# Optimization experiments

Hardware: AMD Instinct MI355X
Metric: run time of the kernel (lower is better)

The kernel has to match this reference:

```python
import jax, jax.numpy as jnp
import numpy as np

N, E = 50000, 800000
H, C = 4, 32          # heads, channels -> concat dim 128
ED = 8                # edge_dim
NREL = 16             # n_relations
LAYERS = 3
MLP_HID = 100
NEG_SLOPE = 0.2


def setup_inputs():
    key = jax.random.key(0)
    ks = jax.random.split(key, 16)
    s = 0.1
    return {
        "x": jax.random.normal(ks[0], (N, 1), jnp.float32),
        "edge_index": jax.random.randint(ks[1], (2, E), 0, N),
        "edge_type": jax.random.randint(ks[2], (E,), 0, NREL),
        "edge_emb": jax.random.normal(ks[3], (NREL, ED), jnp.float32) * s,
        "W_l0": jax.random.normal(ks[4], (C, H * C), jnp.float32) * s,
        "W_l1": jax.random.normal(ks[5], (H * C, H * C), jnp.float32) * s,
        "W_l2": jax.random.normal(ks[6], (H * C, H * C), jnp.float32) * s,
        "att_src": jax.random.normal(ks[7], (LAYERS, H, C), jnp.float32) * s,
        "att_dst": jax.random.normal(ks[8], (LAYERS, H, C), jnp.float32) * s,
        "att_edge": jax.random.normal(ks[9], (LAYERS, H, C), jnp.float32) * s,
        "W_edge": jax.random.normal(ks[10], (LAYERS, ED, H * C), jnp.float32) * s,
        "bias": jax.random.normal(ks[11], (LAYERS, H * C), jnp.float32) * s,
        "mlp_W1": jax.random.normal(ks[12], (H * C, MLP_HID), jnp.float32) * s,
        "mlp_b1": jnp.zeros((MLP_HID,), jnp.float32),
        "mlp_W2": jax.random.normal(ks[13], (MLP_HID, 1), jnp.float32) * s,
        "mlp_b2": jnp.zeros((1,), jnp.float32),
    }


def _gat_layer(x, src, dst, edge_attr, W, a_src, a_dst, a_edge, We, b):
    # PyG GATConv: shared lin for src/dst, additive attention + edge attr term
    n = x.shape[0]
    h = (x @ W).reshape(n, H, C)                      # [N,H,C]
    e = (edge_attr @ We).reshape(-1, H, C)            # [E',H,C]
    s_src = (h * a_src).sum(-1)                       # [N,H]
    s_dst = (h * a_dst).sum(-1)                       # [N,H]
    s_edge = (e * a_edge).sum(-1)                     # [E',H]
    alpha = jax.nn.leaky_relu(s_src[src] + s_dst[dst] + s_edge, NEG_SLOPE)
    # softmax over incoming edges of each destination node
    amax = jax.ops.segment_max(alpha, dst, num_segments=n)
    ealpha = jnp.exp(alpha - amax[dst])
    denom = jax.ops.segment_sum(ealpha, dst, num_segments=n)
    alpha = ealpha / (denom[dst] + 1e-16)             # [E',H]
    msg = h[src] * alpha[:, :, None]                  # [E',H,C]
    out = jax.ops.segment_sum(msg, dst, num_segments=n)
    return out.reshape(n, H * C) + b


def _forward(x, edge_index, edge_type, edge_emb, W_l0, W_l1, W_l2,
             att_src, att_dst, att_edge, W_edge, bias,
             mlp_W1, mlp_b1, mlp_W2, mlp_b2):
    n = x.shape[0]
    x = jnp.broadcast_to(x, (n, C))                   # x.expand(-1, channels)
    src, dst = edge_index[0], edge_index[1]
    loop = jnp.arange(n)
    src_f = jnp.concatenate([src, loop])              # add_self_loops
    dst_f = jnp.concatenate([dst, loop])
    Ws = [W_l0, W_l1, W_l2]
    for i in range(LAYERS):
        edge_attr = edge_emb[edge_type]               # [E,ED]
        fill = jnp.broadcast_to(edge_attr.mean(0), (n, ED))  # fill_value='mean'
        edge_attr_f = jnp.concatenate([edge_attr, fill], axis=0)
        xl = x
        x = _gat_layer(x, src_f, dst_f, edge_attr_f, Ws[i],
                       att_src[i], att_dst[i], att_edge[i], W_edge[i], bias[i])
        if i > 0:
            x = x + xl                                # residual (i>0 only)
        x = jax.nn.relu(x)                            # nonlin; norm='none'
    h = jax.nn.relu(x @ mlp_W1 + mlp_b1)
    return jax.nn.sigmoid(h @ mlp_W2 + mlp_b2)        # [N,1]


def reference(x, edge_index, edge_type, edge_emb, W_l0, W_l1, W_l2,
              att_src, att_dst, att_edge, W_edge, bias,
              mlp_W1, mlp_b1, mlp_W2, mlp_b2):
    return _forward(x, edge_index, edge_type, edge_emb, W_l0, W_l1, W_l2,
                    att_src, att_dst, att_edge, W_edge, bias,
                    mlp_W1, mlp_b1, mlp_W2, mlp_b2)
```

## Files before the change

### kernel.cpp

```cpp
#include <hip/hip_runtime.h>
#include <hip/hip_bf16.h>
#include <hip/hip_fp16.h>

#define HCONC 128
#define NHEAD 4
#define CCH   32
#define EDIM  8
#define NREL  16
#define BCAP  5120
#define TILE  2048

typedef float floatx2 __attribute__((ext_vector_type(2)));
typedef short bf16x8 __attribute__((ext_vector_type(8)));
typedef float f32x4 __attribute__((ext_vector_type(4)));

__device__ inline unsigned short pack_fp8x2(float a, float b) {
    return (unsigned short)(__builtin_amdgcn_cvt_pk_fp8_f32(a, b, 0, false) & 0xFFFF);
}
__device__ inline unsigned pack_bf2(float lo, float hi) {
    __hip_bfloat162 v;
    v.x = __float2bfloat16(lo);
    v.y = __float2bfloat16(hi);
    return *(unsigned*)&v;
}

__global__ __launch_bounds__(256) void binA_kernel(
    const int* __restrict__ ei, const int* __restrict__ etype, int E, int nbuk, int nA,
    int* __restrict__ gcursor, int* __restrict__ cnt, unsigned* __restrict__ ebuf,
    const float* __restrict__ W_l1, const float* __restrict__ W_l2,
    const float* __restrict__ mW1,
    unsigned* __restrict__ Wl1q, unsigned* __restrict__ Wl2q, unsigned* __restrict__ W1q,
    const float* __restrict__ W_l0, const float* __restrict__ emb,
    const float* __restrict__ att_src, const float* __restrict__ att_dst,
    const float* __restrict__ att_edge, const float* __restrict__ W_edge,
    float* __restrict__ W0s, float* __restrict__ SA0, float* __restrict__ SD0,
    float* __restrict__ stab) {
    __shared__ int hist[256], lbase[256], gbase[256], tmp[256];
    __shared__ int lcnt16[NREL];
    __shared__ unsigned srt[TILE];
    __shared__ unsigned char sbuk[TILE];
    __shared__ float W0s_s[HCONC];
    int t = threadIdx.x;

    if ((int)blockIdx.x >= nA) {
        int pb = (int)blockIdx.x - nA;
        if (pb == 92) {
            if (t < HCONC) {
                float s = 0.f;
                for (int k = 0; k < CCH; k++) s += W_l0[k * HCONC + t];
                W0s[t] = s; W0s_s[t] = s;
            }
            __syncthreads();
            if (t < NHEAD) {
                float sa = 0.f, sd = 0.f;
                for (int c = 0; c < CCH; c++) {
                    sa += W0s_s[t * CCH + c] * att_src[t * CCH + c];
                    sd += W0s_s[t * CCH + c] * att_dst[t * CCH + c];
                }
                SA0[t] = sa; SD0[t] = sd;
            }
            if (t < 192) {
                int l = t >> 6, rem = t & 63, typ = rem >> 2, hh = rem & 3;
                const float* attr = emb + typ * EDIM;
                const float* We = W_edge + l * EDIM * HCONC;
                const float* ae = att_edge + l * HCONC + hh * CCH;
                float s = 0.f;
                for (int c = 0; c < CCH; c++) {
                    float ev = 0.f;
                    for (int dd = 0; dd < EDIM; dd++)
                        ev += attr[dd] * We[dd * HCONC + hh * CCH + c];
                    s += ev * ae[c];
                }
                stab[l * 68 + typ * 4 + hh] = s;
            }
            return;
        }
        int i = pb * 256 + t;
        if (i < 16384) {
            const float* W = (i < 8192) ? W_l1 : W_l2;
            unsigned* dst = (i < 8192) ? Wl1q : Wl2q;
            int r = i & 8191;
            int j2 = r & 3, lane = (r >> 2) & 63, kb = (r >> 8) & 3, tt = r >> 10;
            int k0 = kb * 32 + ((lane >> 4) & 3) * 8 + 2 * j2;
            int c = 16 * tt + (lane & 15);
            dst[r] = pack_bf2(W[k0 * 128 + c], W[(k0 + 1) * 128 + c]);
        } else if (i < 16384 + 7168) {
            int r = i - 16384;
            int j2 = r & 3, lane = (r >> 2) & 63, kb = (r >> 8) & 3, tt = r >> 10;
            int k0 = kb * 32 + ((lane >> 4) & 3) * 8 + 2 * j2;
            int c = 16 * tt + (lane & 15);
            float lo = (c < 100) ? mW1[k0 * 100 + c] : 0.f;
            float hi = (c < 100) ? mW1[(k0 + 1) * 100 + c] : 0.f;
            W1q[r] = pack_bf2(lo, hi);
        }
        return;
    }

    hist[t] = 0;
    if (t < NREL) lcnt16[t] = 0;
    __syncthreads();

    int base = blockIdx.x * TILE;
    int count = min(TILE, E - base);

    unsigned rec[8]; int slot[8]; int buk[8];
#pragma unroll
    for (int i = 0; i < 8; i++) {
        int idx = t + i * 256;
        if (idx < count) {
            int g = base + idx;
            int s = ei[g], d = ei[E + g], ty = etype[g];
            rec[i] = (unsigned)s | ((unsigned)ty << 16) | ((unsigned)(d & 255) << 20);
            buk[i] = d >> 8;
            slot[i] = atomicAdd(&hist[buk[i]], 1);
            atomicAdd(&lcnt16[ty], 1);
        } else buk[i] = -1;
    }
    __syncthreads();

    int v = hist[t];
    tmp[t] = v; __syncthreads();
    for (int off = 1; off < 256; off <<= 1) {
        int add = (t >= off) ? tmp[t - off] : 0; __syncthreads();
        tmp[t] += add; __syncthreads();
    }
    lbase[t] = tmp[t] - v;
    if (t < nbuk && v > 0) gbase[t] = atomicAdd(&gcursor[t], v);
    __syncthreads();

#pragma unroll
    for (int i = 0; i < 8; i++)
        if (buk[i] >= 0) {
            int pos = lbase[buk[i]] + slot[i];
            srt[pos] = rec[i];
            sbuk[pos] = (unsigned char)buk[i];
        }
    if (t < NREL) atomicAdd(&cnt[t], lcnt16[t]);
    __syncthreads();

    for (int idx = t; idx < count; idx += 256) {
        unsigned r = srt[idx];
        int bk = sbuk[idx];
        int rel = gbase[bk] + idx - lbase[bk];
        if (rel < BCAP) ebuf[bk * BCAP + rel] = r;
    }
}

__global__ __launch_bounds__(256) void binB_kernel(
    const unsigned* __restrict__ ebuf, const int* __restrict__ gcursor,
    int n, int nbuk,
    int* __restrict__ row_ptr, unsigned* __restrict__ col,
    const int* __restrict__ cnt, float* __restrict__ stab, int E,
    const float* __restrict__ x,
    const float* __restrict__ SA0, const float* __restrict__ SD0,
    float* __restrict__ val0) {
    __shared__ int hist[256], lcur[256], tmp[256];
    __shared__ unsigned colsl[BCAP];
    __shared__ __align__(16) float stab0[68];
    int b = blockIdx.x, t = threadIdx.x;

    if (t < 64) stab0[t] = stab[t];
    float invE = 1.f / (float)E;
    if (t < 4) {
        float s = 0.f;
        for (int r = 0; r < NREL; r++) s += (float)cnt[r] * stab[r * 4 + t];
        stab0[64 + t] = s * invE;
    }

    int c = (t < nbuk) ? gcursor[t] : 0;
    tmp[t] = c; __syncthreads();
    for (int off = 1; off < 256; off <<= 1) {
        int add = (t >= off) ? tmp[t - off] : 0; __syncthreads();
        tmp[t] += add; __syncthreads();
    }
    int gstart = (b == 0) ? 0 : tmp[b - 1];
    if (b == 0 && t == nbuk - 1) row_ptr[n] = tmp[t];
    if (b == 0 && t < 12) {
        int l = t >> 2, hh = t & 3;
        float s = 0.f;
        for (int r = 0; r < NREL; r++) s += (float)cnt[r] * stab[l * 68 + r * 4 + hh];
        stab[l * 68 + 64 + hh] = s * invE;
    }
    __syncthreads();

    int bbase = b * BCAP;
    int cntb = min(gcursor[b], BCAP);
    hist[t] = 0;
    __syncthreads();
    for (int i = t; i < cntb; i += 256) {
        unsigned r = ebuf[bbase + i];
        atomicAdd(&hist[r >> 20], 1);
    }
    __syncthreads();
    int v = hist[t];
    tmp[t] = v; __syncthreads();
    for (int off = 1; off < 256; off <<= 1) {
        int add = (t >= off) ? tmp[t - off] : 0; __syncthreads();
        tmp[t] += add; __syncthreads();
    }
    lcur[t] = tmp[t] - v;
    int gdst = (b << 8) + t;
    if (gdst < n) row_ptr[gdst] = gstart + tmp[t] - v;
    __syncthreads();
    for (int i = t; i < cntb; i += 256) {
        unsigned r = ebuf[bbase + i];
        int pos = atomicAdd(&lcur[r >> 20], 1);
        colsl[pos] = r & 0xFFFFFu;
    }
    __syncthreads();
    for (int i = t; i < cntb; i += 256)
        col[gstart + i] = colsl[i];

    int lo = tmp[t] - v, hi = tmp[t];
    if (gdst < n) {
        float xd = x[gdst];
        float4 sa4 = *(const float4*)SA0;
        float4 sdc = *(const float4*)SD0;
        float sd0 = xd * sdc.x, sd1 = xd * sdc.y, sd2 = xd * sdc.z, sd3 = xd * sdc.w;
        float s0 = fmaf(xd, sa4.x, sd0) + stab0[64];
        float s1 = fmaf(xd, sa4.y, sd1) + stab0[65];
        float s2 = fmaf(xd, sa4.z, sd2) + stab0[66];
        float s3 = fmaf(xd, sa4.w, sd3) + stab0[67];
        s0 = s0 > 0.f ? s0 : 0.2f * s0;
        s1 = s1 > 0.f ? s1 : 0.2f * s1;
        s2 = s2 > 0.f ? s2 : 0.2f * s2;
        s3 = s3 > 0.f ? s3 : 0.2f * s3;
        float w0 = __expf(s0), w1 = __expf(s1), w2 = __expf(s2), w3 = __expf(s3);
        float den0 = w0, den1 = w1, den2 = w2, den3 = w3;
        float sx0 = w0 * xd, sx1 = w1 * xd, sx2 = w2 * xd, sx3 = w3 * xd;
        for (int j = lo; j < hi; j++) {
            unsigned p = colsl[j];
            float xv = x[p & 0xFFFFu];
            int typ = (int)(p >> 16);
            float4 st = *(const float4*)&stab0[typ * 4];
            float e0 = fmaf(xv, sa4.x, sd0) + st.x;
            float e1 = fmaf(xv, sa4.y, sd1) + st.y;
            float e2 = fmaf(xv, sa4.z, sd2) + st.z;
            float e3 = fmaf(xv, sa4.w, sd3) + st.w;
            e0 = e0 > 0.f ? e0 : 0.2f * e0;
            e1 = e1 > 0.f ? e1 : 0.2f * e1;
            e2 = e2 > 0.f ? e2 : 0.2f * e2;
            e3 = e3 > 0.f ? e3 : 0.2f * e3;
            float g0 = __expf(e0), g1 = __expf(e1), g2 = __expf(e2), g3 = __expf(e3);
            den0 += g0; den1 += g1; den2 += g2; den3 += g3;
            sx0 = fmaf(g0, xv, sx0); sx1 = fmaf(g1, xv, sx1);
            sx2 = fmaf(g2, xv, sx2); sx3 = fmaf(g3, xv, sx3);
        }
        float4 vo;
        vo.x = sx0 / (den0 + 1e-16f);
        vo.y = sx1 / (den1 + 1e-16f);
        vo.z = sx2 / (den2 + 1e-16f);
        vo.w = sx3 / (den3 + 1e-16f);
        ((float4*)val0)[gdst] = vo;
    }
}

__global__ __launch_bounds__(256, 2) void transform0_kernel(
    const float* __restrict__ val0, const float* __restrict__ W0s,
    const float* __restrict__ bias0, const unsigned* __restrict__ Wq,
    const float* __restrict__ a_src, const float* __restrict__ a_dst,
    unsigned short* __restrict__ h8, float* __restrict__ s_src,
    float* __restrict__ s_dst, int n) {
    __shared__ unsigned short hs[64 * 128];
    int tid = threadIdx.x;
    int lane = tid & 63;
    int wv = tid >> 6;
    int q = lane >> 4, nl = lane & 15;
    int row_blk = blockIdx.x * 64;
    int wrow = wv * 16;

    int arow = row_blk + wrow + nl;
    if (arow >= n) arow = n - 1;
    float4 v4 = ((const float4*)val0)[arow];

    f32x4 acc[8];
#pragma unroll
    for (int t = 0; t < 8; t++) acc[t] = (f32x4){0.f, 0.f, 0.f, 0.f};

    const uint4* Wp4 = (const uint4*)Wq;
#pragma unroll
    for (int kb = 0; kb < 4; kb++) {
        int c4 = 8 * kb + 2 * q;
        float4 wa = ((const float4*)W0s)[c4];
        float4 wb = ((const float4*)W0s)[c4 + 1];
        float4 ba = ((const float4*)bias0)[c4];
        float4 bb = ((const float4*)bias0)[c4 + 1];
        float vr = kb == 0 ? v4.x : kb == 1 ? v4.y : kb == 2 ? v4.z : v4.w;
        float x0 = fmaxf(fmaf(vr, wa.x, ba.x), 0.f);
        float x1 = fmaxf(fmaf(vr, wa.y, ba.y), 0.f);
        float x2 = fmaxf(fmaf(vr, wa.z, ba.z), 0.f);
        float x3 = fmaxf(fmaf(vr, wa.w, ba.w), 0.f);
        float x4 = fmaxf(fmaf(vr, wb.x, bb.x), 0.f);
        float x5 = fmaxf(fmaf(vr, wb.y, bb.y), 0.f);
        float x6 = fmaxf(fmaf(vr, wb.z, bb.z), 0.f);
        float x7 = fmaxf(fmaf(vr, wb.w, bb.w), 0.f);
        uint4 ua;
        ua.x = pack_bf2(x0, x1);
        ua.y = pack_bf2(x2, x3);
        ua.z = pack_bf2(x4, x5);
        ua.w = pack_bf2(x6, x7);
        bf16x8 af = __builtin_bit_cast(bf16x8, ua);
#pragma unroll
        for (int t = 0; t < 8; t++) {
            uint4 ub = Wp4[(t * 4 + kb) * 64 + lane];
            bf16x8 bf = __builtin_bit_cast(bf16x8, ub);
            acc[t] = __builtin_amdgcn_mfma_f32_16x16x32_bf16(af, bf, acc[t], 0, 0, 0);
        }
    }

    float av[8], dv[8];
#pragma unroll
    for (int t = 0; t < 8; t++) {
        av[t] = a_src[16 * t + nl];
        dv[t] = a_dst[16 * t + nl];
    }
#pragma unroll
    for (int reg = 0; reg < 4; reg++) {
        float t0 = acc[0][reg] * av[0] + acc[1][reg] * av[1];
        float t1 = acc[2][reg] * av[2] + acc[3][reg] * av[3];
        float t2 = acc[4][reg] * av[4] + acc[5][reg] * av[5];
        float t3 = acc[6][reg] * av[6] + acc[7][reg] * av[7];
        float d0 = acc[0][reg] * dv[0] + acc[1][reg] * dv[1];
        float d1 = acc[2][reg] * dv[2] + acc[3][reg] * dv[3];
        float d2 = acc[4][reg] * dv[4] + acc[5][reg] * dv[5];
        float d3 = acc[6][reg] * dv[6] + acc[7][reg] * dv[7];
#pragma unroll
        for (int off = 1; off <= 8; off <<= 1) {
            t0 += __shfl_xor(t0, off); t1 += __shfl_xor(t1, off);
            t2 += __shfl_xor(t2, off); t3 += __shfl_xor(t3, off);
            d0 += __shfl_xor(d0, off); d1 += __shfl_xor(d1, off);
            d2 += __shfl_xor(d2, off); d3 += __shfl_xor(d3, off);
        }
        int row = row_blk + wrow + q * 4 + reg;
        if (row < n && nl < 4) {
            float ts = nl == 0 ? t0 : nl == 1 ? t1 : nl == 2 ? t2 : t3;
            float td = nl == 0 ? d0 : nl == 1 ? d1 : nl == 2 ? d2 : d3;
            s_src[row * 4 + nl] = ts;
            s_dst[row * 4 + nl] = td;
        }
    }

#pragma unroll
    for (int t = 0; t < 8; t++) {
#pragma unroll
        for (int reg = 0; reg < 4; reg++) {
            __hip_bfloat16 b = __float2bfloat16(acc[t][reg]);
            hs[(wrow + q * 4 + reg) * 128 + 16 * t + nl] = *(unsigned short*)&b;
        }
    }
    __syncthreads();
    const unsigned* hsu = (const unsigned*)hs;
#pragma unroll
    for (int i = 0; i < 16; i++) {
        int pidx = tid + i * 256;
        int rl = pidx >> 6, cp = pidx & 63;
        int row = row_blk + rl;
        if (row < n) {
            unsigned u = hsu[rl * 64 + cp];
            float f0 = __uint_as_float(u << 16);
            float f1 = __uint_as_float(u & 0xFFFF0000u);
            h8[(size_t)row * 64 + cp] = pack_fp8x2(f0, f1);
        }
    }
}

__global__ __launch_bounds__(256, 2) void transform_kernel(
    const unsigned short* __restrict__ Xbf, const unsigned* __restrict__ Wq,
    const float* __restrict__ a_src, const float* __restrict__ a_dst,
    unsigned short* __restrict__ h8, float* __restrict__ s_src,
    float* __restrict__ s_dst, int n) {
    __shared__ unsigned short hs[64 * 128];
    int tid = threadIdx.x;
    int lane = tid & 63;
    int wv = tid >> 6;
    int q = lane >> 4, nl = lane & 15;
    int row_blk = blockIdx.x * 64;
    int wrow = wv * 16;

    int arow = row_blk + wrow + nl;
    if (arow >= n) arow = n - 1;
    const uint4* Xr = (const uint4*)(Xbf + (size_t)arow * HCONC);

    f32x4 acc[8];
#pragma unroll
    for (int t = 0; t < 8; t++) acc[t] = (f32x4){0.f, 0.f, 0.f, 0.f};

    const uint4* Wp4 = (const uint4*)Wq;
#pragma unroll
    for (int kb = 0; kb < 4; kb++) {
        uint4 ua = Xr[kb * 4 + q];
        bf16x8 af = __builtin_bit_cast(bf16x8, ua);
#pragma unroll
        for (int t = 0; t < 8; t++) {
            uint4 ub = Wp4[(t * 4 + kb) * 64 + lane];
            bf16x8 bf = __builtin_bit_cast(bf16x8, ub);
            acc[t] = __builtin_amdgcn_mfma_f32_16x16x32_bf16(af, bf, acc[t], 0, 0, 0);
        }
    }

    float av[8], dv[8];
#pragma unroll
    for (int t = 0; t < 8; t++) {
        av[t] = a_src[16 * t + nl];
        dv[t] = a_dst[16 * t + nl];
    }
#pragma unroll
    for (int reg = 0; reg < 4; reg++) {
        float t0 = acc[0][reg] * av[0] + acc[1][reg] * av[1];
        float t1 = acc[2][reg] * av[2] + acc[3][reg] * av[3];
        float t2 = acc[4][reg] * av[4] + acc[5][reg] * av[5];
        float t3 = acc[6][reg] * av[6] + acc[7][reg] * av[7];
        float d0 = acc[0][reg] * dv[0] + acc[1][reg] * dv[1];
        float d1 = acc[2][reg] * dv[2] + acc[3][reg] * dv[3];
        float d2 = acc[4][reg] * dv[4] + acc[5][reg] * dv[5];
        float d3 = acc[6][reg] * dv[6] + acc[7][reg] * dv[7];
#pragma unroll
        for (int off = 1; off <= 8; off <<= 1) {
            t0 += __shfl_xor(t0, off); t1 += __shfl_xor(t1, off);
            t2 += __shfl_xor(t2, off); t3 += __shfl_xor(t3, off);
            d0 += __shfl_xor(d0, off); d1 += __shfl_xor(d1, off);
            d2 += __shfl_xor(d2, off); d3 += __shfl_xor(d3, off);
        }
        int row = row_blk + wrow + q * 4 + reg;
        if (row < n && nl < 4) {
            float ts = nl == 0 ? t0 : nl == 1 ? t1 : nl == 2 ? t2 : t3;
            float td = nl == 0 ? d0 : nl == 1 ? d1 : nl == 2 ? d2 : d3;
            s_src[row * 4 + nl] = ts;
            s_dst[row * 4 + nl] = td;
        }
    }

#pragma unroll
    for (int t = 0; t < 8; t++) {
#pragma unroll
        for (int reg = 0; reg < 4; reg++) {
            __hip_bfloat16 b = __float2bfloat16(acc[t][reg]);
            hs[(wrow + q * 4 + reg) * 128 + 16 * t + nl] = *(unsigned short*)&b;
        }
    }
    __syncthreads();
    const unsigned* hsu = (const unsigned*)hs;
#pragma unroll
    for (int i = 0; i < 16; i++) {
        int pidx = tid + i * 256;
        int rl = pidx >> 6, cp = pidx & 63;
        int row = row_blk + rl;
        if (row < n) {
            unsigned u = hsu[rl * 64 + cp];
            float f0 = __uint_as_float(u << 16);
            float f1 = __uint_as_float(u & 0xFFFF0000u);
            h8[(size_t)row * 64 + cp] = pack_fp8x2(f0, f1);
        }
    }
}

template <bool VAL_RES, bool OUT_BF16, bool RES_BF16>
__global__ __launch_bounds__(256) void agg_kernel(
    const unsigned char* __restrict__ h8,
    const float* __restrict__ s_src, const float* __restrict__ s_dst,
    const int* __restrict__ row_ptr, const unsigned* __restrict__ col,
    const float* __restrict__ tab, const float* __restrict__ bias,
    const void* __restrict__ x_prev,
    const float* __restrict__ val0, const float* __restrict__ W0s,
    const float* __restrict__ bias0,
    void* __restrict__ x_out, int n) {
    __shared__ __align__(16) float stab_s[68];
    if (threadIdx.x < 68) stab_s[threadIdx.x] = tab[threadIdx.x];
    __syncthreads();

    int d = __builtin_amdgcn_readfirstlane(blockIdx.x * 4 + (threadIdx.x >> 6));
    if (d >= n) return;
    int lane = threadIdx.x & 63;
    int strm = lane >> 4;
    int l16 = lane & 15;
    int head = l16 >> 2;

    int start = row_ptr[d], end = row_ptr[d + 1];
    float4 sd4 = ((const float4*)s_dst)[d];

    float den = 0.f;
    float a0 = 0.f, a1 = 0.f, a2 = 0.f, a3 = 0.f;
    float a4 = 0.f, a5 = 0.f, a6 = 0.f, a7 = 0.f;

    if (strm == 0) {
        float sdh = head == 0 ? sd4.x : head == 1 ? sd4.y : head == 2 ? sd4.z : sd4.w;
        float s = s_src[d * 4 + head] + sdh + stab_s[64 + head];
        s = s > 0.f ? s : 0.2f * s;
        float w = __expf(s);
        uint2 u = ((const uint2*)(h8 + (size_t)d * 128))[l16];
        floatx2 f01 = __builtin_amdgcn_cvt_pk_f32_fp8((int)u.x, false);
        floatx2 f23 = __builtin_amdgcn_cvt_pk_f32_fp8((int)u.x, true);
        floatx2 f45 = __builtin_amdgcn_cvt_pk_f32_fp8((int)u.y, false);
        floatx2 f67 = __builtin_amdgcn_cvt_pk_f32_fp8((int)u.y, true);
        den = w;
        a0 = w * f01.x;  a1 = w * f01.y;
        a2 = w * f23.x;  a3 = w * f23.y;
        a4 = w * f45.x;  a5 = w * f45.y;
        a6 = w * f67.x;  a7 = w * f67.y;
    }

    for (int base = start; base < end; base += 64) {
        float4 w4 = make_float4(0.f, 0.f, 0.f, 0.f);
        int esrc = 0;
        int e = base + lane;
        if (e < end) {
            unsigned pp = col[e];
            esrc = (int)(pp & 0xFFFFu);
            int typ = (int)(pp >> 16);
            float4 ss4 = ((const float4*)s_src)[esrc];
            float4 st4 = *(const float4*)&stab_s[typ * 4];
            float s0 = ss4.x + sd4.x + st4.x;
            float s1 = ss4.y + sd4.y + st4.y;
            float s2 = ss4.z + sd4.z + st4.z;
            float s3 = ss4.w + sd4.w + st4.w;
            s0 = s0 > 0.f ? s0 : 0.2f * s0;
            s1 = s1 > 0.f ? s1 : 0.2f * s1;
            s2 = s2 > 0.f ? s2 : 0.2f * s2;
            s3 = s3 > 0.f ? s3 : 0.2f * s3;
            w4.x = __expf(s0); w4.y = __expf(s1);
            w4.z = __expf(s2); w4.w = __expf(s3);
        }
        int C = min(64, end - base);
        int steps = (C + 3) >> 2;
        for (int i = 0; i < steps; i++) {
            int j = i * 4 + strm;
            float wx = __shfl(w4.x, j);
            float wy = __shfl(w4.y, j);
            float wz = __shfl(w4.z, j);
            float ww = __shfl(w4.w, j);
            int sj = __shfl(esrc, j);
            float w = head == 0 ? wx : head == 1 ? wy : head == 2 ? wz : ww;
            uint2 u = ((const uint2*)(h8 + (size_t)sj * 128))[l16];
            floatx2 f01 = __builtin_amdgcn_cvt_pk_f32_fp8((int)u.x, false);
            floatx2 f23 = __builtin_amdgcn_cvt_pk_f32_fp8((int)u.x, true);
            floatx2 f45 = __builtin_amdgcn_cvt_pk_f32_fp8((int)u.y, false);
            floatx2 f67 = __builtin_amdgcn_cvt_pk_f32_fp8((int)u.y, true);
            den += w;
            a0 = fmaf(w, f01.x, a0);  a1 = fmaf(w, f01.y, a1);
            a2 = fmaf(w, f23.x, a2);  a3 = fmaf(w, f23.y, a3);
            a4 = fmaf(w, f45.x, a4);  a5 = fmaf(w, f45.y, a5);
            a6 = fmaf(w, f67.x, a6);  a7 = fmaf(w, f67.y, a7);
        }
    }

#pragma unroll
    for (int off = 16; off <= 32; off <<= 1) {
        den += __shfl_xor(den, off);
        a0 += __shfl_xor(a0, off);  a1 += __shfl_xor(a1, off);
        a2 += __shfl_xor(a2, off);  a3 += __shfl_xor(a3, off);
        a4 += __shfl_xor(a4, off);  a5 += __shfl_xor(a5, off);
        a6 += __shfl_xor(a6, off);  a7 += __shfl_xor(a7, off);
    }

    if (lane < 16) {
        float inv = 1.f / (den + 1e-16f);
        float4 b0 = ((const float4*)bias)[2 * l16];
        float4 b1v = ((const float4*)bias)[2 * l16 + 1];
        float4 o0v, o1v;
        o0v.x = a0 * inv + b0.x;  o0v.y = a1 * inv + b0.y;
        o0v.z = a2 * inv + b0.z;  o0v.w = a3 * inv + b0.w;
        o1v.x = a4 * inv + b1v.x; o1v.y = a5 * inv + b1v.y;
        o1v.z = a6 * inv + b1v.z; o1v.w = a7 * inv + b1v.w;
        if (VAL_RES) {
            float vv = val0[d * 4 + head];
            float4 wa = ((const float4*)W0s)[2 * l16];
            float4 wb = ((const float4*)W0s)[2 * l16 + 1];
            float4 ba = ((const float4*)bias0)[2 * l16];
            float4 bb = ((const float4*)bias0)[2 * l16 + 1];
            o0v.x += fmaxf(fmaf(vv, wa.x, ba.x), 0.f);
            o0v.y += fmaxf(fmaf(vv, wa.y, ba.y), 0.f);
            o0v.z += fmaxf(fmaf(vv, wa.z, ba.z), 0.f);
            o0v.w += fmaxf(fmaf(vv, wa.w, ba.w), 0.f);
            o1v.x += fmaxf(fmaf(vv, wb.x, bb.x), 0.f);
            o1v.y += fmaxf(fmaf(vv, wb.y, bb.y), 0.f);
            o1v.z += fmaxf(fmaf(vv, wb.z, bb.z), 0.f);
            o1v.w += fmaxf(fmaf(vv, wb.w, bb.w), 0.f);
        } else if (RES_BF16) {
            uint4 pk = ((const uint4*)x_prev)[(size_t)d * 16 + l16];
            o0v.x += __uint_as_float(pk.x << 16);
            o0v.y += __uint_as_float(pk.x & 0xFFFF0000u);
            o0v.z += __uint_as_float(pk.y << 16);
            o0v.w += __uint_as_float(pk.y & 0xFFFF0000u);
            o1v.x += __uint_as_float(pk.z << 16);
            o1v.y += __uint_as_float(pk.z & 0xFFFF0000u);
            o1v.z += __uint_as_float(pk.w << 16);
            o1v.w += __uint_as_float(pk.w & 0xFFFF0000u);
        } else if (x_prev) {
            float4 p0 = ((const float4*)x_prev)[(size_t)d * 32 + 2 * l16];
            float4 p1 = ((const float4*)x_prev)[(size_t)d * 32 + 2 * l16 + 1];
            o0v.x += p0.x; o0v.y += p0.y; o0v.z += p0.z; o0v.w += p0.w;
            o1v.x += p1.x; o1v.y += p1.y; o1v.z += p1.z; o1v.w += p1.w;
        }
        o0v.x = fmaxf(o0v.x, 0.f); o0v.y = fmaxf(o0v.y, 0.f);
        o0v.z = fmaxf(o0v.z, 0.f); o0v.w = fmaxf(o0v.w, 0.f);
        o1v.x = fmaxf(o1v.x, 0.f); o1v.y = fmaxf(o1v.y, 0.f);
        o1v.z = fmaxf(o1v.z, 0.f); o1v.w = fmaxf(o1v.w, 0.f);
        if (OUT_BF16) {
            uint4 pk;
            pk.x = pack_bf2(o0v.x, o0v.y);
            pk.y = pack_bf2(o0v.z, o0v.w);
            pk.z = pack_bf2(o1v.x, o1v.y);
            pk.w = pack_bf2(o1v.z, o1v.w);
            ((uint4*)x_out)[(size_t)d * 16 + l16] = pk;
        } else {
            ((float4*)x_out)[(size_t)d * 32 + 2 * l16]     = o0v;
            ((float4*)x_out)[(size_t)d * 32 + 2 * l16 + 1] = o1v;
        }
    }
}

__global__ __launch_bounds__(256, 2) void mlp_kernel(
    const unsigned short* __restrict__ Xbf, const unsigned* __restrict__ W1q,
    const float* __restrict__ b1, const float* __restrict__ W2,
    const float* __restrict__ b2, float* __restrict__ out, int n) {
    int tid = threadIdx.x;
    int lane = tid & 63;
    int wv = tid >> 6;
    int q = lane >> 4, nl = lane & 15;
    int row_blk = blockIdx.x * 64;
    int wrow = wv * 16;

    int arow = row_blk + wrow + nl;
    if (arow >= n) arow = n - 1;
    const uint4* Xr = (const uint4*)(Xbf + (size_t)arow * HCONC);

    f32x4 acc[7];
#pragma unroll
    for (int t = 0; t < 7; t++) acc[t] = (f32x4){0.f, 0.f, 0.f, 0.f};

    const uint4* Wp4 = (const uint4*)W1q;
#pragma unroll
    for (int kb = 0; kb < 4; kb++) {
        uint4 ua = Xr[kb * 4 + q];
        bf16x8 af = __builtin_bit_cast(bf16x8, ua);
#pragma unroll
        for (int t = 0; t < 7; t++) {
            uint4 ub = Wp4[(t * 4 + kb) * 64 + lane];
            bf16x8 bf = __builtin_bit_cast(bf16x8, ub);
            acc[t] = __builtin_amdgcn_mfma_f32_16x16x32_bf16(af, bf, acc[t], 0, 0, 0);
        }
    }

    float b1c[7], w2c[7];
#pragma unroll
    for (int t = 0; t < 7; t++) {
        int c = 16 * t + nl;
        bool vld = c < 100;
        b1c[t] = vld ? b1[c] : 0.f;
        w2c[t] = vld ? W2[c] : 0.f;
    }
    float b2v = b2[0];

#pragma unroll
    for (int reg = 0; reg < 4; reg++) {
        float sum = 0.f;
#pragma unroll
        for (int t = 0; t < 7; t++) {
            float hv = fmaxf(acc[t][reg] + b1c[t], 0.f);
            sum = fmaf(hv, w2c[t], sum);
        }
#pragma unroll
        for (int off = 1; off <= 8; off <<= 1)
            sum += __shfl_xor(sum, off);
        int row = row_blk + wrow + q * 4 + reg;
        if (nl == 0 && row < n)
            out[row] = 1.f / (1.f + __expf(-(sum + b2v)));
    }
}

extern "C" void kernel_launch(void* const* d_in, const int* in_sizes, int n_in,
                              void* d_out, int out_size, void* d_ws, size_t ws_size,
                              hipStream_t stream) {
    const float* x       = (const float*)d_in[0];
    const int*   ei      = (const int*)d_in[1];
    const int*   etype   = (const int*)d_in[2];
    const float* emb     = (const float*)d_in[3];
    const float* W_l0    = (const float*)d_in[4];
    const float* W_l1    = (const float*)d_in[5];
    const float* W_l2    = (const float*)d_in[6];
    const float* att_src = (const float*)d_in[7];
    const float* att_dst = (const float*)d_in[8];
    const float* att_edge= (const float*)d_in[9];
    const float* W_edge  = (const float*)d_in[10];
    const float* bias    = (const float*)d_in[11];
    const float* mW1     = (const float*)d_in[12];
    const float* mb1     = (const float*)d_in[13];
    const float* mW2     = (const float*)d_in[14];
    const float* mb2     = (const float*)d_in[15];

    int n = in_sizes[0];
    int E = in_sizes[2];
    int nbuk = (n + 255) >> 8;
    int nA = (E + TILE - 1) / TILE;

    float* p   = (float*)d_ws;
    float* xa  = p; p += (size_t)n * HCONC;
    float* xb  = p; p += (size_t)n * HCONC;
    float* ssrc = p; p += (size_t)n * NHEAD;
    float* sdst = p; p += (size_t)n * NHEAD;
    float* val0 = p; p += (size_t)n * NHEAD;
    float* hbf  = p; p += (size_t)n * 32;
    unsigned* Wl1q = (unsigned*)p; p += 8192;
    unsigned* Wl2q = (unsigned*)p; p += 8192;
    unsigned* W1q  = (unsigned*)p; p += 7168;
    int* row_ptr     = (int*)p;
    int* gcursor     = row_ptr + n + 1;
    int* cnt         = gcursor + 256;
    float* W0s    = (float*)(cnt + 16);
    float* SA0    = W0s + HCONC;
    float* SD0    = SA0 + NHEAD;
    float* meanat = SD0 + NHEAD;
    float* stab   = meanat + EDIM;
    char* raw = (char*)(stab + 256);
    unsigned* ebuf = (unsigned*)(((uintptr_t)raw + 15) & ~(uintptr_t)15);
    unsigned* col = ebuf + (size_t)nbuk * BCAP;

    hipMemsetAsync(gcursor, 0, (256 + 16) * sizeof(int), stream);
    binA_kernel<<<nA + 93, 256, 0, stream>>>(ei, etype, E, nbuk, nA, gcursor, cnt,
                                             ebuf, W_l1, W_l2, mW1, Wl1q, Wl2q, W1q,
                                             W_l0, emb, att_src, att_dst, att_edge,
                                             W_edge, W0s, SA0, SD0, stab);
    binB_kernel<<<nbuk, 256, 0, stream>>>(ebuf, gcursor, n, nbuk, row_ptr, col,
                                          cnt, stab, E, x, SA0, SD0, val0);

    transform0_kernel<<<(n + 63) / 64, 256, 0, stream>>>(val0, W0s, bias + 0, Wl1q,
                                                         att_src + 128, att_dst + 128,
                                                         (unsigned short*)hbf, ssrc, sdst, n);
    agg_kernel<true, true, false><<<(n + 3) / 4, 256, 0, stream>>>(
        (const unsigned char*)hbf, ssrc, sdst, row_ptr, col,
        stab + 68, bias + 128, nullptr, val0, W0s, bias + 0, xb, n);
    transform_kernel<<<(n + 63) / 64, 256, 0, stream>>>((const unsigned short*)xb, Wl2q,
                                                        att_src + 256, att_dst + 256,
                                                        (unsigned short*)hbf, ssrc, sdst, n);
    agg_kernel<false, true, true><<<(n + 3) / 4, 256, 0, stream>>>(
        (const unsigned char*)hbf, ssrc, sdst, row_ptr, col,
        stab + 136, bias + 256, xb, nullptr, nullptr, nullptr, xa, n);
    mlp_kernel<<<(n + 63) / 64, 256, 0, stream>>>((const unsigned short*)xa, W1q,
                                                  mb1, mW2, mb2, (float*)d_out, n);
}
```

Measured before the change: 242.3 us.

## Assign one 16-lane group per destination node in GAT aggregation

The aggregation kernel now maps each destination node to a 16-lane group instead of a full 64-lane wavefront, so one wave handles four nodes and each block handles sixteen. Each lane computes its own head's attention weight per edge directly, with no cooperative weight precompute, shuffles or cross-stream reductions. This removes shuffle and reduction overhead and the lanes left idle on low-degree nodes. In exchange, attention scores are recomputed redundantly across the lanes of a head, edge loads are serial within a group, and groups in one wave can diverge when their nodes have different degrees. The unused fp32 residual branch was also dropped.

```diff
diff --git a/kernel.cpp b/kernel.cpp
--- a/kernel.cpp
+++ b/kernel.cpp
@@ -468,144 +468,99 @@
     if (threadIdx.x < 68) stab_s[threadIdx.x] = tab[threadIdx.x];
     __syncthreads();
 
-    int d = __builtin_amdgcn_readfirstlane(blockIdx.x * 4 + (threadIdx.x >> 6));
-    if (d >= n) return;
-    int lane = threadIdx.x & 63;
-    int strm = lane >> 4;
+    int tid = threadIdx.x;
+    int lane = tid & 63;
+    int grp = lane >> 4;
     int l16 = lane & 15;
     int head = l16 >> 2;
+    int d = blockIdx.x * 16 + (tid >> 6) * 4 + grp;
+    if (d >= n) return;
 
     int start = row_ptr[d], end = row_ptr[d + 1];
-    float4 sd4 = ((const float4*)s_dst)[d];
-
-    float den = 0.f;
-    float a0 = 0.f, a1 = 0.f, a2 = 0.f, a3 = 0.f;
-    float a4 = 0.f, a5 = 0.f, a6 = 0.f, a7 = 0.f;
-
-    if (strm == 0) {
-        float sdh = head == 0 ? sd4.x : head == 1 ? sd4.y : head == 2 ? sd4.z : sd4.w;
-        float s = s_src[d * 4 + head] + sdh + stab_s[64 + head];
-        s = s > 0.f ? s : 0.2f * s;
-        float w = __expf(s);
-        uint2 u = ((const uint2*)(h8 + (size_t)d * 128))[l16];
-        floatx2 f01 = __builtin_amdgcn_cvt_pk_f32_fp8((int)u.x, false);
-        floatx2 f23 = __builtin_amdgcn_cvt_pk_f32_fp8((int)u.x, true);
-        floatx2 f45 = __builtin_amdgcn_cvt_pk_f32_fp8((int)u.y, false);
-        floatx2 f67 = __builtin_amdgcn_cvt_pk_f32_fp8((int)u.y, true);
-        den = w;
-        a0 = w * f01.x;  a1 = w * f01.y;
-        a2 = w * f23.x;  a3 = w * f23.y;
-        a4 = w * f45.x;  a5 = w * f45.y;
-        a6 = w * f67.x;  a7 = w * f67.y;
-    }
-
-    for (int base = start; base < end; base += 64) {
-        float4 w4 = make_float4(0.f, 0.f, 0.f, 0.f);
-        int esrc = 0;
-        int e = base + lane;
-        if (e < end) {
-            unsigned pp = col[e];
-            esrc = (int)(pp & 0xFFFFu);
-            int typ = (int)(pp >> 16);
-            float4 ss4 = ((const float4*)s_src)[esrc];
-            float4 st4 = *(const float4*)&stab_s[typ * 4];
-            float s0 = ss4.x + sd4.x + st4.x;
-            float s1 = ss4.y + sd4.y + st4.y;
-            float s2 = ss4.z + sd4.z + st4.z;
-            float s3 = ss4.w + sd4.w + st4.w;
-            s0 = s0 > 0.f ? s0 : 0.2f * s0;
-            s1 = s1 > 0.f ? s1 : 0.2f * s1;
-            s2 = s2 > 0.f ? s2 : 0.2f * s2;
-            s3 = s3 > 0.f ? s3 : 0.2f * s3;
-            w4.x = __expf(s0); w4.y = __expf(s1);
-            w4.z = __expf(s2); w4.w = __expf(s3);
-        }
-        int C = min(64, end - base);
-        int steps = (C + 3) >> 2;
-        for (int i = 0; i < steps; i++) {
-            int j = i * 4 + strm;
-            float wx = __shfl(w4.x, j);
-            float wy = __shfl(w4.y, j);
-            float wz = __shfl(w4.z, j);
-            float ww = __shfl(w4.w, j);
-            int sj = __shfl(esrc, j);
-            float w = head == 0 ? wx : head == 1 ? wy : head == 2 ? wz : ww;
-            uint2 u = ((const uint2*)(h8 + (size_t)sj * 128))[l16];
-            floatx2 f01 = __builtin_amdgcn_cvt_pk_f32_fp8((int)u.x, false);
-            floatx2 f23 = __builtin_amdgcn_cvt_pk_f32_fp8((int)u.x, true);
-            floatx2 f45 = __builtin_amdgcn_cvt_pk_f32_fp8((int)u.y, false);
-            floatx2 f67 = __builtin_amdgcn_cvt_pk_f32_fp8((int)u.y, true);
-            den += w;
-            a0 = fmaf(w, f01.x, a0);  a1 = fmaf(w, f01.y, a1);
-            a2 = fmaf(w, f23.x, a2);  a3 = fmaf(w, f23.y, a3);
-            a4 = fmaf(w, f45.x, a4);  a5 = fmaf(w, f45.y, a5);
-            a6 = fmaf(w, f67.x, a6);  a7 = fmaf(w, f67.y, a7);
-        }
-    }
-
-#pragma unroll
-    for (int off = 16; off <= 32; off <<= 1) {
-        den += __shfl_xor(den, off);
-        a0 += __shfl_xor(a0, off);  a1 += __shfl_xor(a1, off);
-        a2 += __shfl_xor(a2, off);  a3 += __shfl_xor(a3, off);
-        a4 += __shfl_xor(a4, off);  a5 += __shfl_xor(a5, off);
-        a6 += __shfl_xor(a6, off);  a7 += __shfl_xor(a7, off);
-    }
-
-    if (lane < 16) {
-        float inv = 1.f / (den + 1e-16f);
-        float4 b0 = ((const float4*)bias)[2 * l16];
-        float4 b1v = ((const float4*)bias)[2 * l16 + 1];
-        float4 o0v, o1v;
-        o0v.x = a0 * inv + b0.x;  o0v.y = a1 * inv + b0.y;
-        o0v.z = a2 * inv + b0.z;  o0v.w = a3 * inv + b0.w;
-        o1v.x = a4 * inv + b1v.x; o1v.y = a5 * inv + b1v.y;
-        o1v.z = a6 * inv + b1v.z; o1v.w = a7 * inv + b1v.w;
-        if (VAL_RES) {
-            float vv = val0[d * 4 + head];
-            float4 wa = ((const float4*)W0s)[2 * l16];
-            float4 wb = ((const float4*)W0s)[2 * l16 + 1];
-            float4 ba = ((const float4*)bias0)[2 * l16];
-            float4 bb = ((const float4*)bias0)[2 * l16 + 1];
-            o0v.x += fmaxf(fmaf(vv, wa.x, ba.x), 0.f);
-            o0v.y += fmaxf(fmaf(vv, wa.y, ba.y), 0.f);
-            o0v.z += fmaxf(fmaf(vv, wa.z, ba.z), 0.f);
-            o0v.w += fmaxf(fmaf(vv, wa.w, ba.w), 0.f);
-            o1v.x += fmaxf(fmaf(vv, wb.x, bb.x), 0.f);
-            o1v.y += fmaxf(fmaf(vv, wb.y, bb.y), 0.f);
-            o1v.z += fmaxf(fmaf(vv, wb.z, bb.z), 0.f);
-            o1v.w += fmaxf(fmaf(vv, wb.w, bb.w), 0.f);
-        } else if (RES_BF16) {
-            uint4 pk = ((const uint4*)x_prev)[(size_t)d * 16 + l16];
-            o0v.x += __uint_as_float(pk.x << 16);
-            o0v.y += __uint_as_float(pk.x & 0xFFFF0000u);
-            o0v.z += __uint_as_float(pk.y << 16);
-            o0v.w += __uint_as_float(pk.y & 0xFFFF0000u);
-            o1v.x += __uint_as_float(pk.z << 16);
-            o1v.y += __uint_as_float(pk.z & 0xFFFF0000u);
-            o1v.z += __uint_as_float(pk.w << 16);
-            o1v.w += __uint_as_float(pk.w & 0xFFFF0000u);
-        } else if (x_prev) {
-            float4 p0 = ((const float4*)x_prev)[(size_t)d * 32 + 2 * l16];
-            float4 p1 = ((const float4*)x_prev)[(size_t)d * 32 + 2 * l16 + 1];
-            o0v.x += p0.x; o0v.y += p0.y; o0v.z += p0.z; o0v.w += p0.w;
-            o1v.x += p1.x; o1v.y += p1.y; o1v.z += p1.z; o1v.w += p1.w;
-        }
-        o0v.x = fmaxf(o0v.x, 0.f); o0v.y = fmaxf(o0v.y, 0.f);
-        o0v.z = fmaxf(o0v.z, 0.f); o0v.w = fmaxf(o0v.w, 0.f);
-        o1v.x = fmaxf(o1v.x, 0.f); o1v.y = fmaxf(o1v.y, 0.f);
-        o1v.z = fmaxf(o1v.z, 0.f); o1v.w = fmaxf(o1v.w, 0.f);
-        if (OUT_BF16) {
-            uint4 pk;
-            pk.x = pack_bf2(o0v.x, o0v.y);
-            pk.y = pack_bf2(o0v.z, o0v.w);
-            pk.z = pack_bf2(o1v.x, o1v.y);
-            pk.w = pack_bf2(o1v.z, o1v.w);
-            ((uint4*)x_out)[(size_t)d * 16 + l16] = pk;
-        } else {
-            ((float4*)x_out)[(size_t)d * 32 + 2 * l16]     = o0v;
-            ((float4*)x_out)[(size_t)d * 32 + 2 * l16 + 1] = o1v;
-        }
+    float sdh = s_dst[d * 4 + head];
+
+    float s = s_src[d * 4 + head] + sdh + stab_s[64 + head];
+    s = s > 0.f ? s : 0.2f * s;
+    float w = __expf(s);
+    uint2 u = ((const uint2*)(h8 + (size_t)d * 128))[l16];
+    floatx2 f01 = __builtin_amdgcn_cvt_pk_f32_fp8((int)u.x, false);
+    floatx2 f23 = __builtin_amdgcn_cvt_pk_f32_fp8((int)u.x, true);
+    floatx2 f45 = __builtin_amdgcn_cvt_pk_f32_fp8((int)u.y, false);
+    floatx2 f67 = __builtin_amdgcn_cvt_pk_f32_fp8((int)u.y, true);
+    float den = w;
+    float a0 = w * f01.x, a1 = w * f01.y;
+    float a2 = w * f23.x, a3 = w * f23.y;
+    float a4 = w * f45.x, a5 = w * f45.y;
+    float a6 = w * f67.x, a7 = w * f67.y;
+
+#pragma unroll 4
+    for (int e = start; e < end; e++) {
+        unsigned pp = col[e];
+        int esrc = (int)(pp & 0xFFFFu);
+        int typ = (int)(pp >> 16);
+        float ss = s_src[esrc * 4 + head];
+        float sc = ss + sdh + stab_s[typ * 4 + head];
+        sc = sc > 0.f ? sc : 0.2f * sc;
+        float we = __expf(sc);
+        uint2 ue = ((const uint2*)(h8 + (size_t)esrc * 128))[l16];
+        floatx2 g01 = __builtin_amdgcn_cvt_pk_f32_fp8((int)ue.x, false);
+        floatx2 g23 = __builtin_amdgcn_cvt_pk_f32_fp8((int)ue.x, true);
+        floatx2 g45 = __builtin_amdgcn_cvt_pk_f32_fp8((int)ue.y, false);
+        floatx2 g67 = __builtin_amdgcn_cvt_pk_f32_fp8((int)ue.y, true);
+        den += we;
+        a0 = fmaf(we, g01.x, a0);  a1 = fmaf(we, g01.y, a1);
+        a2 = fmaf(we, g23.x, a2);  a3 = fmaf(we, g23.y, a3);
+        a4 = fmaf(we, g45.x, a4);  a5 = fmaf(we, g45.y, a5);
+        a6 = fmaf(we, g67.x, a6);  a7 = fmaf(we, g67.y, a7);
+    }
+
+    float inv = 1.f / (den + 1e-16f);
+    float4 b0 = ((const float4*)bias)[2 * l16];
+    float4 b1v = ((const float4*)bias)[2 * l16 + 1];
+    float4 o0v, o1v;
+    o0v.x = a0 * inv + b0.x;  o0v.y = a1 * inv + b0.y;
+    o0v.z = a2 * inv + b0.z;  o0v.w = a3 * inv + b0.w;
+    o1v.x = a4 * inv + b1v.x; o1v.y = a5 * inv + b1v.y;
+    o1v.z = a6 * inv + b1v.z; o1v.w = a7 * inv + b1v.w;
+    if (VAL_RES) {
+        float vv = val0[d * 4 + head];
+        float4 wa = ((const float4*)W0s)[2 * l16];
+        float4 wb = ((const float4*)W0s)[2 * l16 + 1];
+        float4 ba = ((const float4*)bias0)[2 * l16];
+        float4 bb = ((const float4*)bias0)[2 * l16 + 1];
+        o0v.x += fmaxf(fmaf(vv, wa.x, ba.x), 0.f);
+        o0v.y += fmaxf(fmaf(vv, wa.y, ba.y), 0.f);
+        o0v.z += fmaxf(fmaf(vv, wa.z, ba.z), 0.f);
+        o0v.w += fmaxf(fmaf(vv, wa.w, ba.w), 0.f);
+        o1v.x += fmaxf(fmaf(vv, wb.x, bb.x), 0.f);
+        o1v.y += fmaxf(fmaf(vv, wb.y, bb.y), 0.f);
+        o1v.z += fmaxf(fmaf(vv, wb.z, bb.z), 0.f);
+        o1v.w += fmaxf(fmaf(vv, wb.w, bb.w), 0.f);
+    } else if (RES_BF16) {
+        uint4 pk = ((const uint4*)x_prev)[(size_t)d * 16 + l16];
+        o0v.x += __uint_as_float(pk.x << 16);
+        o0v.y += __uint_as_float(pk.x & 0xFFFF0000u);
+        o0v.z += __uint_as_float(pk.y << 16);
+        o0v.w += __uint_as_float(pk.y & 0xFFFF0000u);
+        o1v.x += __uint_as_float(pk.z << 16);
+        o1v.y += __uint_as_float(pk.z & 0xFFFF0000u);
+        o1v.z += __uint_as_float(pk.w << 16);
+        o1v.w += __uint_as_float(pk.w & 0xFFFF0000u);
+    }
+    o0v.x = fmaxf(o0v.x, 0.f); o0v.y = fmaxf(o0v.y, 0.f);
+    o0v.z = fmaxf(o0v.z, 0.f); o0v.w = fmaxf(o0v.w, 0.f);
+    o1v.x = fmaxf(o1v.x, 0.f); o1v.y = fmaxf(o1v.y, 0.f);
+    o1v.z = fmaxf(o1v.z, 0.f); o1v.w = fmaxf(o1v.w, 0.f);
+    if (OUT_BF16) {
+        uint4 pk;
+        pk.x = pack_bf2(o0v.x, o0v.y);
+        pk.y = pack_bf2(o0v.z, o0v.w);
+        pk.z = pack_bf2(o1v.x, o1v.y);
+        pk.w = pack_bf2(o1v.z, o1v.w);
+        ((uint4*)x_out)[(size_t)d * 16 + l16] = pk;
+    } else {
+        ((float4*)x_out)[(size_t)d * 32 + 2 * l16]     = o0v;
+        ((float4*)x_out)[(size_t)d * 32 + 2 * l16 + 1] = o1v;
     }
 }
 
@@ -726,13 +681,13 @@
     transform0_kernel<<<(n + 63) / 64, 256, 0, stream>>>(val0, W0s, bias + 0, Wl1q,
                                                          att_src + 128, att_dst + 128,
                                                          (unsigned short*)hbf, ssrc, sdst, n);
-    agg_kernel<true, true, false><<<(n + 3) / 4, 256, 0, stream>>>(
+    agg_kernel<true, true, false><<<(n + 15) / 16, 256, 0, stream>>>(
         (const unsigned char*)hbf, ssrc, sdst, row_ptr, col,
         stab + 68, bias + 128, nullptr, val0, W0s, bias + 0, xb, n);
     transform_kernel<<<(n + 63) / 64, 256, 0, stream>>>((const unsigned short*)xb, Wl2q,
                                                         att_src + 256, att_dst + 256,
                                                         (unsigned short*)hbf, ssrc, sdst, n);
-    agg_kernel<false, true, true><<<(n + 3) / 4, 256, 0, stream>>>(
+    agg_kernel<false, true, true><<<(n + 15) / 16, 256, 0, stream>>>(
         (const unsigned char*)hbf, ssrc, sdst, row_ptr, col,
         stab + 136, bias + 256, xb, nullptr, nullptr, nullptr, xa, n);
     mlp_kernel<<<(n + 63) / 64, 256, 0, stream>>>((const unsigned short*)xa, W1q,
```

Result: faster. 220.4 us (-9.0%).
